# Kernel tuning notes

Measured on AMD Instinct MI355X. Metric: run time of the kernel, lower is better.

## Reference

```python
import jax, jax.numpy as jnp
import numpy as np

GN_GROUPS = 32
GN_EPS = 1e-5


def conv1x1(x, w, b):
    # x: [B,C,H,W], w: [O,C], b: [O]
    return jnp.einsum('bchw,oc->bohw', x, w) + b[None, :, None, None]


def maxpool2(x):
    B, C, H, W = x.shape
    return x.reshape(B, C, H // 2, 2, W // 2, 2).max(axis=(3, 5))


def group_norm(x, w, b, groups=GN_GROUPS, eps=GN_EPS):
    B, C, H, W = x.shape
    xg = x.reshape(B, groups, -1)
    m = xg.mean(axis=-1, keepdims=True)
    v = xg.var(axis=-1, keepdims=True)
    xn = ((xg - m) * jax.lax.rsqrt(v + eps)).reshape(B, C, H, W)
    return xn * w[None, :, None, None] + b[None, :, None, None]


def setup_inputs() -> dict:
    key = jax.random.key(0)
    ks = jax.random.split(key, 8)
    B, C, Ci, H, W = 4, 128, 64, 96, 96
    s_in = 1.0 / np.sqrt(C)
    s_ic = 1.0 / np.sqrt(Ci)
    return {
        'x': jax.random.normal(ks[0], (B, C, H, W), jnp.float32),
        'w_theta': jax.random.normal(ks[1], (Ci, C), jnp.float32) * s_in,
        'b_theta': jnp.zeros((Ci,), jnp.float32),
        'w_phi': jax.random.normal(ks[2], (Ci, C), jnp.float32) * s_in,
        'b_phi': jnp.zeros((Ci,), jnp.float32),
        'w_g': jax.random.normal(ks[3], (Ci, C), jnp.float32) * s_in,
        'b_g': jnp.zeros((Ci,), jnp.float32),
        'w_W': jax.random.normal(ks[4], (C, Ci), jnp.float32) * s_ic,
        'b_W': jnp.zeros((C,), jnp.float32),
        'gn_w': jnp.ones((C,), jnp.float32),
        'gn_b': jnp.zeros((C,), jnp.float32),
    }


def reference(x, w_theta, b_theta, w_phi, b_phi, w_g, b_g, w_W, b_W, gn_w, gn_b):
    B, C, H, W = x.shape
    Ci = w_theta.shape[0]
    # projections (1x1 convs); phi and g are 2x2 max-pooled (sub_sample=True)
    theta = conv1x1(x, w_theta, b_theta).reshape(B, Ci, H * W)          # [B,Ci,N]
    phi = maxpool2(conv1x1(x, w_phi, b_phi)).reshape(B, Ci, -1)         # [B,Ci,N']
    g = maxpool2(conv1x1(x, w_g, b_g)).reshape(B, Ci, -1)               # [B,Ci,N']
    # unscaled single-head attention
    f = jnp.einsum('bcn,bcm->bnm', theta, phi)                          # [B,N,N']
    f = jax.nn.softmax(f, axis=-1)
    y = jnp.einsum('bnm,bcm->bcn', f, g).reshape(B, Ci, H, W)           # [B,Ci,H,W]
    w_y = group_norm(conv1x1(y, w_W, b_W), gn_w, gn_b)
    return w_y + x
```

## Files before the change

### kernel.cpp

```cpp
#include <hip/hip_runtime.h>
#include <math.h>

#define B_ 4
#define C_ 128
#define CI_ 64
#define H_ 96
#define W_ 96
#define HW_ (H_*W_)
#define NP_ 2304
#define GROUPS_ 32
#define EPS_ 1e-5f
#define KVT_ 32
#define NT_ (NP_/KVT_)

typedef _Float16 f16x8 __attribute__((ext_vector_type(8)));
typedef _Float16 f16x2 __attribute__((ext_vector_type(2)));
typedef __attribute__((ext_vector_type(4))) float f32x4;

__device__ inline f32x4 mfma16h(f16x8 a, f16x8 b, f32x4 c) {
    return __builtin_amdgcn_mfma_f32_16x16x32_f16(a, b, c, 0, 0, 0);
}
__device__ inline float h2f(unsigned short s) {
    return (float)__builtin_bit_cast(_Float16, s);
}
__device__ inline unsigned pk_f16(float a, float b) {
    return __builtin_bit_cast(unsigned, __builtin_amdgcn_cvt_pkrtz(a, b));
}
__device__ inline f16x8 pk8(float v0, float v1, float v2, float v3,
                            float v4, float v5, float v6, float v7) {
    uint4 u = { pk_f16(v0, v1), pk_f16(v2, v3), pk_f16(v4, v5), pk_f16(v6, v7) };
    return __builtin_bit_cast(f16x8, u);
}
__device__ inline void gload_lds16(const void* g, void* l) {
    __builtin_amdgcn_global_load_lds(
        (const __attribute__((address_space(1))) void*)reinterpret_cast<uintptr_t>(g),
        (__attribute__((address_space(3))) void*)(unsigned)reinterpret_cast<uintptr_t>(l),
        16, 0, 0);
}

__global__ __launch_bounds__(256) void wprep_kernel(
    const float* __restrict__ w_theta, const float* __restrict__ w_phi,
    const float* __restrict__ w_g,     const float* __restrict__ w_W,
    unsigned short* __restrict__ Whall)
{
    const int idx = blockIdx.x * 256 + threadIdx.x;
    float v;
    if      (idx <  8192) v = w_theta[idx];
    else if (idx < 16384) v = w_phi[idx - 8192];
    else if (idx < 24576) v = w_g[idx - 16384];
    else                  v = w_W[idx - 24576];
    Whall[idx] = __builtin_bit_cast(unsigned short, (_Float16)v);
}

__global__ __launch_bounds__(256) void proj_kernel(
    const float* __restrict__ x, const unsigned short* __restrict__ Whall,
    const float* __restrict__ b_theta, const float* __restrict__ b_phi,
    const float* __restrict__ b_g,
    unsigned short* __restrict__ Qo, unsigned short* __restrict__ phiF,
    unsigned short* __restrict__ gF)
{
    __shared__ __align__(16) unsigned short pb[4][16 * 72];

    const int t    = threadIdx.x;
    const int wv   = t >> 6;
    const int lane = t & 63;
    const int lr   = lane & 15;
    const int lg   = lane >> 4;
    const int b    = blockIdx.y;
    const int px0  = blockIdx.x * 64 + wv * 16;

    const float* xb = x + (size_t)b * C_ * HW_ + px0 + lr;
    f16x8 xa[4];
    #pragma unroll
    for (int u = 0; u < 4; ++u) {
        const float* p = xb + (size_t)(u * 32 + lg * 8) * HW_;
        xa[u] = pk8(p[0], p[(size_t)HW_], p[2 * (size_t)HW_], p[3 * (size_t)HW_],
                    p[4 * (size_t)HW_], p[5 * (size_t)HW_], p[6 * (size_t)HW_],
                    p[7 * (size_t)HW_]);
    }

    #pragma unroll
    for (int mat = 0; mat < 3; ++mat) {
        const unsigned short* Whp = Whall + mat * 8192;
        const float* bsel = (mat == 0) ? b_theta : (mat == 1) ? b_phi : b_g;
        unsigned short* osel = (mat == 0) ? Qo : (mat == 1) ? phiF : gF;

        f32x4 D[4];
        #pragma unroll
        for (int ct = 0; ct < 4; ++ct) D[ct] = (f32x4){0.f, 0.f, 0.f, 0.f};
        #pragma unroll
        for (int u = 0; u < 4; ++u)
            #pragma unroll
            for (int ct = 0; ct < 4; ++ct) {
                f16x8 wb = *(const f16x8*)&Whp[(ct * 16 + lr) * 128 + u * 32 + lg * 8];
                D[ct] = mfma16h(xa[u], wb, D[ct]);
            }

        #pragma unroll
        for (int ct = 0; ct < 4; ++ct) {
            const float bi = bsel[ct * 16 + lr];
            #pragma unroll
            for (int r2 = 0; r2 < 4; ++r2)
                pb[wv][(4 * lg + r2) * 72 + ct * 16 + lr] =
                    __builtin_bit_cast(unsigned short, (_Float16)(D[ct][r2] + bi));
        }
        {
            const int px = lane >> 2, ch = lane & 3;
            f16x8 y0 = *(const f16x8*)&pb[wv][px * 72 + ch * 16];
            f16x8 y1 = *(const f16x8*)&pb[wv][px * 72 + ch * 16 + 8];
            unsigned short* op = osel + ((size_t)b * HW_ + px0 + px) * CI_ + ch * 16;
            *(f16x8*)op       = y0;
            *(f16x8*)(op + 8) = y1;
        }
    }
}

__global__ __launch_bounds__(256) void pool_kernel(
    const unsigned short* __restrict__ phiF, const unsigned short* __restrict__ gF,
    unsigned short* __restrict__ Ko, unsigned short* __restrict__ Vt)
{
    const int t   = threadIdx.x;
    const int b   = blockIdx.y;
    const int mat = blockIdx.z;
    const int idx = blockIdx.x * 256 + t;
    int m, ci;
    if (mat == 0) { m = idx >> 6; ci = idx & 63; }
    else          { ci = idx / NP_; m = idx - ci * NP_; }
    const int ph = m / 48, pw = m % 48;
    const int n00 = (ph * 2) * W_ + pw * 2;
    const unsigned short* src = mat ? gF : phiF;
    const unsigned short* p = src + ((size_t)b * HW_ + n00) * CI_ + ci;
    float v = fmaxf(fmaxf(h2f(p[0]), h2f(p[CI_])),
                    fmaxf(h2f(p[(size_t)W_ * CI_]), h2f(p[(size_t)(W_ + 1) * CI_])));
    unsigned short r = __builtin_bit_cast(unsigned short, (_Float16)v);
    if (mat == 0) {
        Ko[((size_t)b * NP_ + m) * CI_ + ci] = r;
    } else {
        const int ms = (m & ~31) | (8 * ((m >> 2) & 3) + 4 * ((m >> 4) & 1) + (m & 3));
        Vt[((size_t)b * CI_ + ci) * NP_ + ms] = r;
    }
}

__global__ __launch_bounds__(128) void attn_kernel(
    const unsigned short* __restrict__ Qg, const unsigned short* __restrict__ Kg,
    const unsigned short* __restrict__ Vt, unsigned short* __restrict__ Yh)
{
    __shared__ unsigned char Klds[2][4096];
    __shared__ unsigned char Vlds[2][4096];

    const int t    = threadIdx.x;
    const int wv   = t >> 6;
    const int lane = t & 63;
    const int lr   = lane & 15;
    const int lg   = lane >> 4;
    const int b    = blockIdx.y;
    const int q0   = blockIdx.x * 32 + wv * 16;

    const int krow = lane >> 3;
    const int kchk = (lane & 7) ^ krow;
    const int vrow = lane >> 2;
    const int vchk = (lane & 3) ^ (vrow & 3);

    const unsigned short* Kb = Kg + (size_t)b * NP_ * CI_;
    const unsigned short* Vb = Vt + (size_t)b * CI_ * NP_;

    f16x8 qf[2];
    #pragma unroll
    for (int u = 0; u < 2; ++u)
        qf[u] = *(const f16x8*)(Qg + ((size_t)b * HW_ + q0 + lr) * CI_ + u * 32 + lg * 8);

    f32x4 o_acc[4];
    #pragma unroll
    for (int dt = 0; dt < 4; ++dt) o_acc[dt] = (f32x4){0.f, 0.f, 0.f, 0.f};
    float mrun = -1e30f, lrun = 0.f;

#define STAGE(BUF, TT)                                                          \
    {                                                                           \
        const int kv0_ = (TT) * KVT_;                                           \
        if (wv == 0) {                                                          \
            _Pragma("unroll")                                                   \
            for (int i = 0; i < 4; ++i)                                         \
                gload_lds16(Kb + (size_t)(kv0_ + 8 * i + krow) * CI_ + kchk * 8,\
                            &Klds[BUF][i * 1024]);                              \
        } else {                                                                \
            _Pragma("unroll")                                                   \
            for (int i = 0; i < 4; ++i)                                         \
                gload_lds16(Vb + (size_t)(16 * i + vrow) * NP_ + kv0_ + vchk * 8,\
                            &Vlds[BUF][i * 1024]);                              \
        }                                                                       \
    }

#define COMPUTE(BUF)                                                            \
    {                                                                           \
        f16x8 kf[2][2];                                                         \
        _Pragma("unroll")                                                       \
        for (int u = 0; u < 2; ++u)                                             \
            _Pragma("unroll")                                                   \
            for (int k4 = 0; k4 < 2; ++k4)                                      \
                kf[u][k4] = *(const f16x8*)&Klds[BUF][(k4 * 16 + lr) * 128      \
                                + (((4 * u + lg) ^ (lr & 7)) << 4)];            \
        f32x4 s[2];                                                             \
        s[0] = (f32x4){0.f, 0.f, 0.f, 0.f};                                     \
        s[1] = (f32x4){0.f, 0.f, 0.f, 0.f};                                     \
        __builtin_amdgcn_s_setprio(1);                                          \
        _Pragma("unroll")                                                       \
        for (int u = 0; u < 2; ++u) {                                           \
            s[0] = mfma16h(kf[u][0], qf[u], s[0]);                              \
            s[1] = mfma16h(kf[u][1], qf[u], s[1]);                              \
        }                                                                       \
        __builtin_amdgcn_s_setprio(0);                                          \
        float tmax = fmaxf(fmaxf(fmaxf(s[0][0], s[0][1]),                       \
                                 fmaxf(s[0][2], s[0][3])),                      \
                           fmaxf(fmaxf(s[1][0], s[1][1]),                       \
                                 fmaxf(s[1][2], s[1][3])));                     \
        if (!__all(tmax <= mrun + 8.0f)) {                                      \
            tmax = fmaxf(tmax, __shfl_xor(tmax, 16));                           \
            tmax = fmaxf(tmax, __shfl_xor(tmax, 32));                           \
            const float mnew = fmaxf(mrun, tmax);                               \
            const float sc = __expf(mrun - mnew);                               \
            lrun *= sc;                                                         \
            _Pragma("unroll")                                                   \
            for (int r2 = 0; r2 < 4; ++r2) {                                    \
                const float scb = __shfl(sc, 4 * lg + r2);                      \
                _Pragma("unroll")                                               \
                for (int dt = 0; dt < 4; ++dt) o_acc[dt][r2] *= scb;            \
            }                                                                   \
            mrun = mnew;                                                        \
        }                                                                       \
        const float e00 = __expf(s[0][0] - mrun);                               \
        const float e01 = __expf(s[0][1] - mrun);                               \
        const float e02 = __expf(s[0][2] - mrun);                               \
        const float e03 = __expf(s[0][3] - mrun);                               \
        const float e10 = __expf(s[1][0] - mrun);                               \
        const float e11 = __expf(s[1][1] - mrun);                               \
        const float e12 = __expf(s[1][2] - mrun);                               \
        const float e13 = __expf(s[1][3] - mrun);                               \
        lrun += ((e00 + e01) + (e02 + e03)) + ((e10 + e11) + (e12 + e13));      \
        f16x8 pf = pk8(e00, e01, e02, e03, e10, e11, e12, e13);                 \
        __builtin_amdgcn_s_setprio(1);                                          \
        _Pragma("unroll")                                                       \
        for (int dt = 0; dt < 4; ++dt) {                                        \
            const int vrow_ = dt * 16 + lr;                                     \
            f16x8 vf = *(const f16x8*)&Vlds[BUF][vrow_ * 64                     \
                            + (((lg ^ (lr & 3))) << 4)];                        \
            o_acc[dt] = mfma16h(pf, vf, o_acc[dt]);                             \
        }                                                                       \
        __builtin_amdgcn_s_setprio(0);                                          \
    }

    STAGE(0, 0);
    STAGE(1, 1);

    for (int it = 0; it < NT_ / 2; ++it) {
        const int t0 = 2 * it;
        asm volatile("s_waitcnt vmcnt(4)" ::: "memory");
        __builtin_amdgcn_s_barrier();
        COMPUTE(0);
        __builtin_amdgcn_s_barrier();
        if (t0 + 2 < NT_) STAGE(0, t0 + 2);
        if (it == NT_ / 2 - 1) {
            asm volatile("s_waitcnt vmcnt(0)" ::: "memory");
        } else {
            asm volatile("s_waitcnt vmcnt(4)" ::: "memory");
        }
        __builtin_amdgcn_s_barrier();
        COMPUTE(1);
        __builtin_amdgcn_s_barrier();
        if (t0 + 3 < NT_) STAGE(1, t0 + 3);
    }

    float lt = lrun;
    lt += __shfl_xor(lt, 16);
    lt += __shfl_xor(lt, 32);
    unsigned short* yb = (unsigned short*)&Klds[wv][0];
    #pragma unroll
    for (int r2 = 0; r2 < 4; ++r2) {
        const float inv = 1.0f / __shfl(lt, 4 * lg + r2);
        #pragma unroll
        for (int dt = 0; dt < 4; ++dt)
            yb[(4 * lg + r2) * 72 + dt * 16 + lr] =
                __builtin_bit_cast(unsigned short, (_Float16)(o_acc[dt][r2] * inv));
    }
    {
        const int px = lane >> 2, ch = lane & 3;
        f16x8 y0 = *(const f16x8*)&yb[px * 72 + ch * 16];
        f16x8 y1 = *(const f16x8*)&yb[px * 72 + ch * 16 + 8];
        unsigned short* op = Yh + ((size_t)b * HW_ + q0 + px) * CI_ + ch * 16;
        *(f16x8*)op       = y0;
        *(f16x8*)(op + 8) = y1;
    }
#undef STAGE
#undef COMPUTE
}

__global__ __launch_bounds__(256) void conv2_kernel(
    const unsigned short* __restrict__ Yh, const unsigned short* __restrict__ wWh,
    const float* __restrict__ bW, float* __restrict__ Zg, float* __restrict__ gpart)
{
    __shared__ float wpart[4][32][2];

    const int t    = threadIdx.x;
    const int wv   = t >> 6;
    const int lane = t & 63;
    const int lr   = lane & 15;
    const int lg   = lane >> 4;
    const int b    = blockIdx.y;
    const int n0   = blockIdx.x * 64 + wv * 16;

    f16x8 ya[2];
    #pragma unroll
    for (int u = 0; u < 2; ++u)
        ya[u] = *(const f16x8*)(Yh + ((size_t)b * HW_ + n0 + lr) * CI_ + u * 32 + lg * 8);

    float* Zb = Zg + (size_t)b * C_ * HW_ + n0 + lr;
    #pragma unroll
    for (int ot = 0; ot < 8; ++ot) {
        f32x4 D = (f32x4){0.f, 0.f, 0.f, 0.f};
        #pragma unroll
        for (int u = 0; u < 2; ++u) {
            f16x8 wa = *(const f16x8*)&wWh[(ot * 16 + lr) * CI_ + u * 32 + lg * 8];
            D = mfma16h(wa, ya[u], D);
        }
        float zs = 0.f, zq = 0.f;
        #pragma unroll
        for (int r2 = 0; r2 < 4; ++r2) {
            const int o = ot * 16 + 4 * lg + r2;
            const float z = D[r2] + bW[o];
            Zb[(size_t)o * HW_] = z;
            zs += z;
            zq += z * z;
        }
        zs += __shfl_xor(zs, 1);  zq += __shfl_xor(zq, 1);
        zs += __shfl_xor(zs, 2);  zq += __shfl_xor(zq, 2);
        zs += __shfl_xor(zs, 4);  zq += __shfl_xor(zq, 4);
        zs += __shfl_xor(zs, 8);  zq += __shfl_xor(zq, 8);
        if (lr == 0) {
            wpart[wv][ot * 4 + lg][0] = zs;
            wpart[wv][ot * 4 + lg][1] = zq;
        }
    }
    __syncthreads();
    if (t < 64) {
        const int g = t >> 1, w = t & 1;
        const float v = wpart[0][g][w] + wpart[1][g][w]
                      + wpart[2][g][w] + wpart[3][g][w];
        gpart[(((size_t)b * 144 + blockIdx.x) * 32 + g) * 2 + w] = v;
    }
}

__global__ __launch_bounds__(256) void final_kernel(
    const float* __restrict__ Zg, const float* __restrict__ xg,
    const float* __restrict__ gpart, const float* __restrict__ gnw,
    const float* __restrict__ gnb, float* __restrict__ out)
{
    __shared__ float red[256][2];
    const int t = threadIdx.x;
    const int c = blockIdx.x;
    const int b = blockIdx.y;
    const int g = c >> 2;

    float v1 = 0.f, v2 = 0.f;
    if (t < 144) {
        v1 = gpart[(((size_t)b * 144 + t) * 32 + g) * 2 + 0];
        v2 = gpart[(((size_t)b * 144 + t) * 32 + g) * 2 + 1];
    }
    red[t][0] = v1; red[t][1] = v2;
    __syncthreads();
    for (int off = 128; off > 0; off >>= 1) {
        if (t < off) { red[t][0] += red[t + off][0]; red[t][1] += red[t + off][1]; }
        __syncthreads();
    }
    const float invn = 1.0f / (4 * HW_);
    const float mean = red[0][0] * invn;
    const float var  = red[0][1] * invn - mean * mean;
    const float rstd = rsqrtf(var + EPS_);
    const float sc = rstd * gnw[c];
    const float sh = gnb[c] - mean * sc;

    const float4* zp = (const float4*)(Zg + ((size_t)b * C_ + c) * HW_);
    const float4* xp = (const float4*)(xg + ((size_t)b * C_ + c) * HW_);
    float4*       op = (float4*)(out + ((size_t)b * C_ + c) * HW_);
    #pragma unroll
    for (int i = 0; i < HW_ / 4 / 256; ++i) {
        const int j = i * 256 + t;
        const float4 z  = zp[j];
        const float4 xv = xp[j];
        float4 o;
        o.x = z.x * sc + sh + xv.x;
        o.y = z.y * sc + sh + xv.y;
        o.z = z.z * sc + sh + xv.z;
        o.w = z.w * sc + sh + xv.w;
        op[j] = o;
    }
}

extern "C" void kernel_launch(void* const* d_in, const int* in_sizes, int n_in,
                              void* d_out, int out_size, void* d_ws, size_t ws_size,
                              hipStream_t stream)
{
    const float* x       = (const float*)d_in[0];
    const float* w_theta = (const float*)d_in[1];
    const float* b_theta = (const float*)d_in[2];
    const float* w_phi   = (const float*)d_in[3];
    const float* b_phi   = (const float*)d_in[4];
    const float* w_g     = (const float*)d_in[5];
    const float* b_g     = (const float*)d_in[6];
    const float* w_W     = (const float*)d_in[7];
    const float* b_W     = (const float*)d_in[8];
    const float* gn_w    = (const float*)d_in[9];
    const float* gn_b    = (const float*)d_in[10];
    float* out = (float*)d_out;
    char* wsb  = (char*)d_ws;

    unsigned short* Q    = (unsigned short*)(wsb);
    unsigned short* K    = (unsigned short*)(wsb +  4718592);
    unsigned short* Vt   = (unsigned short*)(wsb +  5898240);
    unsigned short* phiF = (unsigned short*)(wsb +  7077888);
    unsigned short* gF   = (unsigned short*)(wsb + 11796480);
    unsigned short* Yh   = (unsigned short*)(wsb +  7077888);
    float* gpart         = (float*)(wsb + 11796480);
    float* Z             = (float*)(wsb + 16515072);
    unsigned short* Whall= (unsigned short*)(wsb + 35390464);
    unsigned short* wWh  = Whall + 24576;

    wprep_kernel<<<128, 256, 0, stream>>>(w_theta, w_phi, w_g, w_W, Whall);
    proj_kernel <<<dim3(HW_ / 64, B_), 256, 0, stream>>>(
        x, Whall, b_theta, b_phi, b_g, Q, phiF, gF);
    pool_kernel <<<dim3(NP_ * CI_ / 256, B_, 2), 256, 0, stream>>>(phiF, gF, K, Vt);
    attn_kernel <<<dim3(HW_ / 32, B_), 128, 0, stream>>>(Q, K, Vt, Yh);
    conv2_kernel<<<dim3(HW_ / 64, B_), 256, 0, stream>>>(Yh, wWh, b_W, Z, gpart);
    final_kernel<<<dim3(C_, B_), 256, 0, stream>>>(Z, x, gpart, gn_w, gn_b, out);
}
```

Before: 117.0 us.

## Split attention KV range across wave pairs and store conv output as fp16

The attention kernel now runs 256 threads per block. Two wave pairs each handle half of the pooled key/value sequence (36 tiles each) for the same 32 queries. The partial softmax states (running max, sum, output) are merged through LDS at the end, a split-K style flash-decoding combine that shortens each wave's serial loop and adds parallelism. Separately, the conv output Z is stored as fp16 instead of fp32, which halves the traffic between conv2 and the final GroupNorm kernel at some cost in precision.

```diff
diff --git a/kernel.cpp b/kernel.cpp
--- a/kernel.cpp
+++ b/kernel.cpp
@@ -12,6 +12,7 @@
 #define EPS_ 1e-5f
 #define KVT_ 32
 #define NT_ (NP_/KVT_)
+#define TPH_ 36
 
 typedef _Float16 f16x8 __attribute__((ext_vector_type(8)));
 typedef _Float16 f16x2 __attribute__((ext_vector_type(2)));
@@ -141,20 +142,21 @@
     }
 }
 
-__global__ __launch_bounds__(128) void attn_kernel(
+__global__ __launch_bounds__(256) void attn_kernel(
     const unsigned short* __restrict__ Qg, const unsigned short* __restrict__ Kg,
     const unsigned short* __restrict__ Vt, unsigned short* __restrict__ Yh)
 {
-    __shared__ unsigned char Klds[2][4096];
-    __shared__ unsigned char Vlds[2][4096];
+    __shared__ __align__(16) unsigned char KV[2][2][2][4096];
 
     const int t    = threadIdx.x;
     const int wv   = t >> 6;
+    const int qh   = wv >> 1;
+    const int p    = wv & 1;
     const int lane = t & 63;
     const int lr   = lane & 15;
     const int lg   = lane >> 4;
     const int b    = blockIdx.y;
-    const int q0   = blockIdx.x * 32 + wv * 16;
+    const int q0   = blockIdx.x * 32;
 
     const int krow = lane >> 3;
     const int kchk = (lane & 7) ^ krow;
@@ -167,26 +169,27 @@
     f16x8 qf[2];
     #pragma unroll
     for (int u = 0; u < 2; ++u)
-        qf[u] = *(const f16x8*)(Qg + ((size_t)b * HW_ + q0 + lr) * CI_ + u * 32 + lg * 8);
+        qf[u] = *(const f16x8*)(Qg
+            + ((size_t)b * HW_ + q0 + qh * 16 + lr) * CI_ + u * 32 + lg * 8);
 
     f32x4 o_acc[4];
     #pragma unroll
     for (int dt = 0; dt < 4; ++dt) o_acc[dt] = (f32x4){0.f, 0.f, 0.f, 0.f};
     float mrun = -1e30f, lrun = 0.f;
 
-#define STAGE(BUF, TT)                                                          \
+#define STAGE(BUF, TL)                                                          \
     {                                                                           \
-        const int kv0_ = (TT) * KVT_;                                           \
-        if (wv == 0) {                                                          \
+        const int kv0_ = (p * TPH_ + (TL)) * KVT_;                              \
+        if (qh == 0) {                                                          \
             _Pragma("unroll")                                                   \
             for (int i = 0; i < 4; ++i)                                         \
                 gload_lds16(Kb + (size_t)(kv0_ + 8 * i + krow) * CI_ + kchk * 8,\
-                            &Klds[BUF][i * 1024]);                              \
+                            &KV[p][BUF][0][i * 1024]);                          \
         } else {                                                                \
             _Pragma("unroll")                                                   \
             for (int i = 0; i < 4; ++i)                                         \
                 gload_lds16(Vb + (size_t)(16 * i + vrow) * NP_ + kv0_ + vchk * 8,\
-                            &Vlds[BUF][i * 1024]);                              \
+                            &KV[p][BUF][1][i * 1024]);                          \
         }                                                                       \
     }
 
@@ -197,7 +200,7 @@
         for (int u = 0; u < 2; ++u)                                             \
             _Pragma("unroll")                                                   \
             for (int k4 = 0; k4 < 2; ++k4)                                      \
-                kf[u][k4] = *(const f16x8*)&Klds[BUF][(k4 * 16 + lr) * 128      \
+                kf[u][k4] = *(const f16x8*)&KV[p][BUF][0][(k4 * 16 + lr) * 128  \
                                 + (((4 * u + lg) ^ (lr & 7)) << 4)];            \
         f32x4 s[2];                                                             \
         s[0] = (f32x4){0.f, 0.f, 0.f, 0.f};                                     \
@@ -241,7 +244,7 @@
         _Pragma("unroll")                                                       \
         for (int dt = 0; dt < 4; ++dt) {                                        \
             const int vrow_ = dt * 16 + lr;                                     \
-            f16x8 vf = *(const f16x8*)&Vlds[BUF][vrow_ * 64                     \
+            f16x8 vf = *(const f16x8*)&KV[p][BUF][1][vrow_ * 64                 \
                             + (((lg ^ (lr & 3))) << 4)];                        \
             o_acc[dt] = mfma16h(pf, vf, o_acc[dt]);                             \
         }                                                                       \
@@ -251,14 +254,14 @@
     STAGE(0, 0);
     STAGE(1, 1);
 
-    for (int it = 0; it < NT_ / 2; ++it) {
+    for (int it = 0; it < TPH_ / 2; ++it) {
         const int t0 = 2 * it;
         asm volatile("s_waitcnt vmcnt(4)" ::: "memory");
         __builtin_amdgcn_s_barrier();
         COMPUTE(0);
         __builtin_amdgcn_s_barrier();
-        if (t0 + 2 < NT_) STAGE(0, t0 + 2);
-        if (it == NT_ / 2 - 1) {
+        if (t0 + 2 < TPH_) STAGE(0, t0 + 2);
+        if (it == TPH_ / 2 - 1) {
             asm volatile("s_waitcnt vmcnt(0)" ::: "memory");
         } else {
             asm volatile("s_waitcnt vmcnt(4)" ::: "memory");
@@ -266,28 +269,51 @@
         __builtin_amdgcn_s_barrier();
         COMPUTE(1);
         __builtin_amdgcn_s_barrier();
-        if (t0 + 3 < NT_) STAGE(1, t0 + 3);
-    }
+        if (t0 + 3 < TPH_) STAGE(1, t0 + 3);
+    }
+
+    float* cb   = (float*)&KV[0][0][0][0];
+    float* Olds = cb;
+    float* mlb  = cb + 2 * 32 * 68;
 
     float lt = lrun;
     lt += __shfl_xor(lt, 16);
     lt += __shfl_xor(lt, 32);
-    unsigned short* yb = (unsigned short*)&Klds[wv][0];
-    #pragma unroll
-    for (int r2 = 0; r2 < 4; ++r2) {
-        const float inv = 1.0f / __shfl(lt, 4 * lg + r2);
-        #pragma unroll
-        for (int dt = 0; dt < 4; ++dt)
-            yb[(4 * lg + r2) * 72 + dt * 16 + lr] =
-                __builtin_bit_cast(unsigned short, (_Float16)(o_acc[dt][r2] * inv));
-    }
+    if (lg == 0) {
+        mlb[(p * 32 + qh * 16 + lr) * 2 + 0] = mrun;
+        mlb[(p * 32 + qh * 16 + lr) * 2 + 1] = lt;
+    }
+    __syncthreads();
+
     {
-        const int px = lane >> 2, ch = lane & 3;
-        f16x8 y0 = *(const f16x8*)&yb[px * 72 + ch * 16];
-        f16x8 y1 = *(const f16x8*)&yb[px * 72 + ch * 16 + 8];
-        unsigned short* op = Yh + ((size_t)b * HW_ + q0 + px) * CI_ + ch * 16;
-        *(f16x8*)op       = y0;
-        *(f16x8*)(op + 8) = y1;
+        const int row = qh * 16 + lr;
+        const float mg = fmaxf(mlb[(row) * 2 + 0], mlb[(32 + row) * 2 + 0]);
+        const float fac = __expf(mrun - mg);
+        #pragma unroll
+        for (int r2 = 0; r2 < 4; ++r2) {
+            const float fb = __shfl(fac, 4 * lg + r2);
+            #pragma unroll
+            for (int dt = 0; dt < 4; ++dt)
+                Olds[(p * 32 + qh * 16 + 4 * lg + r2) * 68 + dt * 16 + lr]
+                    = o_acc[dt][r2] * fb;
+        }
+    }
+    __syncthreads();
+
+    {
+        const int row = t >> 3;
+        const int c0  = (t & 7) * 8;
+        const float m0 = mlb[row * 2 + 0],  l0 = mlb[row * 2 + 1];
+        const float m1 = mlb[(32 + row) * 2 + 0], l1 = mlb[(32 + row) * 2 + 1];
+        const float mg = fmaxf(m0, m1);
+        const float inv = 1.0f / (l0 * __expf(m0 - mg) + l1 * __expf(m1 - mg));
+        const float* o0 = &Olds[row * 68 + c0];
+        const float* o1 = &Olds[(32 + row) * 68 + c0];
+        float a[8];
+        #pragma unroll
+        for (int i = 0; i < 8; ++i) a[i] = (o0[i] + o1[i]) * inv;
+        f16x8 y = pk8(a[0], a[1], a[2], a[3], a[4], a[5], a[6], a[7]);
+        *(f16x8*)(Yh + ((size_t)b * HW_ + q0 + row) * CI_ + c0) = y;
     }
 #undef STAGE
 #undef COMPUTE
@@ -295,7 +321,8 @@
 
 __global__ __launch_bounds__(256) void conv2_kernel(
     const unsigned short* __restrict__ Yh, const unsigned short* __restrict__ wWh,
-    const float* __restrict__ bW, float* __restrict__ Zg, float* __restrict__ gpart)
+    const float* __restrict__ bW, unsigned short* __restrict__ Zh,
+    float* __restrict__ gpart)
 {
     __shared__ float wpart[4][32][2];
 
@@ -312,7 +339,7 @@
     for (int u = 0; u < 2; ++u)
         ya[u] = *(const f16x8*)(Yh + ((size_t)b * HW_ + n0 + lr) * CI_ + u * 32 + lg * 8);
 
-    float* Zb = Zg + (size_t)b * C_ * HW_ + n0 + lr;
+    unsigned short* Zb = Zh + (size_t)b * C_ * HW_ + n0 + lr;
     #pragma unroll
     for (int ot = 0; ot < 8; ++ot) {
         f32x4 D = (f32x4){0.f, 0.f, 0.f, 0.f};
@@ -326,7 +353,7 @@
         for (int r2 = 0; r2 < 4; ++r2) {
             const int o = ot * 16 + 4 * lg + r2;
             const float z = D[r2] + bW[o];
-            Zb[(size_t)o * HW_] = z;
+            Zb[(size_t)o * HW_] = __builtin_bit_cast(unsigned short, (_Float16)z);
             zs += z;
             zq += z * z;
         }
@@ -349,7 +376,7 @@
 }
 
 __global__ __launch_bounds__(256) void final_kernel(
-    const float* __restrict__ Zg, const float* __restrict__ xg,
+    const unsigned short* __restrict__ Zh, const float* __restrict__ xg,
     const float* __restrict__ gpart, const float* __restrict__ gnw,
     const float* __restrict__ gnb, float* __restrict__ out)
 {
@@ -377,19 +404,19 @@
     const float sc = rstd * gnw[c];
     const float sh = gnb[c] - mean * sc;
 
-    const float4* zp = (const float4*)(Zg + ((size_t)b * C_ + c) * HW_);
+    const unsigned short* zp = Zh + ((size_t)b * C_ + c) * HW_;
     const float4* xp = (const float4*)(xg + ((size_t)b * C_ + c) * HW_);
     float4*       op = (float4*)(out + ((size_t)b * C_ + c) * HW_);
     #pragma unroll
     for (int i = 0; i < HW_ / 4 / 256; ++i) {
         const int j = i * 256 + t;
-        const float4 z  = zp[j];
+        const ushort4 zv = *(const ushort4*)(zp + (size_t)j * 4);
         const float4 xv = xp[j];
         float4 o;
-        o.x = z.x * sc + sh + xv.x;
-        o.y = z.y * sc + sh + xv.y;
-        o.z = z.z * sc + sh + xv.z;
-        o.w = z.w * sc + sh + xv.w;
+        o.x = h2f(zv.x) * sc + sh + xv.x;
+        o.y = h2f(zv.y) * sc + sh + xv.y;
+        o.z = h2f(zv.z) * sc + sh + xv.z;
+        o.w = h2f(zv.w) * sc + sh + xv.w;
         op[j] = o;
     }
 }
@@ -419,7 +446,7 @@
     unsigned short* gF   = (unsigned short*)(wsb + 11796480);
     unsigned short* Yh   = (unsigned short*)(wsb +  7077888);
     float* gpart         = (float*)(wsb + 11796480);
-    float* Z             = (float*)(wsb + 16515072);
+    unsigned short* Zh   = (unsigned short*)(wsb + 16515072);
     unsigned short* Whall= (unsigned short*)(wsb + 35390464);
     unsigned short* wWh  = Whall + 24576;
 
@@ -427,7 +454,7 @@
     proj_kernel <<<dim3(HW_ / 64, B_), 256, 0, stream>>>(
         x, Whall, b_theta, b_phi, b_g, Q, phiF, gF);
     pool_kernel <<<dim3(NP_ * CI_ / 256, B_, 2), 256, 0, stream>>>(phiF, gF, K, Vt);
-    attn_kernel <<<dim3(HW_ / 32, B_), 128, 0, stream>>>(Q, K, Vt, Yh);
-    conv2_kernel<<<dim3(HW_ / 64, B_), 256, 0, stream>>>(Yh, wWh, b_W, Z, gpart);
-    final_kernel<<<dim3(C_, B_), 256, 0, stream>>>(Z, x, gpart, gn_w, gn_b, out);
-}
+    attn_kernel <<<dim3(HW_ / 32, B_), 256, 0, stream>>>(Q, K, Vt, Yh);
+    conv2_kernel<<<dim3(HW_ / 64, B_), 256, 0, stream>>>(Yh, wWh, b_W, Zh, gpart);
+    final_kernel<<<dim3(C_, B_), 256, 0, stream>>>(Zh, x, gpart, gn_w, gn_b, out);
+}
```

Measured after the change: 118.5 us. About the same (+1.3%).

## Double attention KV tile to 64 and store conv2 output in fp16

Applied to the files above, without the earlier changes.

The attention kernel now stages 64 keys and values per tile instead of 32. It uses a unified 128-byte-row XOR swizzle for K and V in LDS and issues four QK and two PV MFMAs per tile, which halves the number of barriers and online-softmax rescale checks. Separately, the pre-GroupNorm conv output Z is written as fp16 rather than fp32, halving its write and read traffic between conv2 and the final kernel. Costs are doubled LDS use per block, which may lower occupancy, and extra rounding error in Z before normalization.

```diff
diff --git a/kernel.cpp b/kernel.cpp
--- a/kernel.cpp
+++ b/kernel.cpp
@@ -10,8 +10,8 @@
 #define NP_ 2304
 #define GROUPS_ 32
 #define EPS_ 1e-5f
-#define KVT_ 32
-#define NT_ (NP_/KVT_)
+#define KVT_ 64
+#define NTT_ (NP_/KVT_)
 
 typedef _Float16 f16x8 __attribute__((ext_vector_type(8)));
 typedef _Float16 f16x2 __attribute__((ext_vector_type(2)));
@@ -145,8 +145,8 @@
     const unsigned short* __restrict__ Qg, const unsigned short* __restrict__ Kg,
     const unsigned short* __restrict__ Vt, unsigned short* __restrict__ Yh)
 {
-    __shared__ unsigned char Klds[2][4096];
-    __shared__ unsigned char Vlds[2][4096];
+    __shared__ __align__(16) unsigned char Klds[2][8192];
+    __shared__ __align__(16) unsigned char Vlds[2][8192];
 
     const int t    = threadIdx.x;
     const int wv   = t >> 6;
@@ -156,10 +156,8 @@
     const int b    = blockIdx.y;
     const int q0   = blockIdx.x * 32 + wv * 16;
 
-    const int krow = lane >> 3;
-    const int kchk = (lane & 7) ^ krow;
-    const int vrow = lane >> 2;
-    const int vchk = (lane & 3) ^ (vrow & 3);
+    const int srow = lane >> 3;
+    const int schk = (lane & 7) ^ srow;
 
     const unsigned short* Kb = Kg + (size_t)b * NP_ * CI_;
     const unsigned short* Vb = Vt + (size_t)b * CI_ * NP_;
@@ -179,40 +177,42 @@
         const int kv0_ = (TT) * KVT_;                                           \
         if (wv == 0) {                                                          \
             _Pragma("unroll")                                                   \
-            for (int i = 0; i < 4; ++i)                                         \
-                gload_lds16(Kb + (size_t)(kv0_ + 8 * i + krow) * CI_ + kchk * 8,\
+            for (int i = 0; i < 8; ++i)                                         \
+                gload_lds16(Kb + (size_t)(kv0_ + 8 * i + srow) * CI_ + schk * 8,\
                             &Klds[BUF][i * 1024]);                              \
         } else {                                                                \
             _Pragma("unroll")                                                   \
-            for (int i = 0; i < 4; ++i)                                         \
-                gload_lds16(Vb + (size_t)(16 * i + vrow) * NP_ + kv0_ + vchk * 8,\
+            for (int i = 0; i < 8; ++i)                                         \
+                gload_lds16(Vb + (size_t)(8 * i + srow) * NP_ + kv0_ + schk * 8,\
                             &Vlds[BUF][i * 1024]);                              \
         }                                                                       \
     }
 
 #define COMPUTE(BUF)                                                            \
     {                                                                           \
-        f16x8 kf[2][2];                                                         \
+        f16x8 kf[2][4];                                                         \
         _Pragma("unroll")                                                       \
         for (int u = 0; u < 2; ++u)                                             \
             _Pragma("unroll")                                                   \
-            for (int k4 = 0; k4 < 2; ++k4)                                      \
+            for (int k4 = 0; k4 < 4; ++k4)                                      \
                 kf[u][k4] = *(const f16x8*)&Klds[BUF][(k4 * 16 + lr) * 128      \
                                 + (((4 * u + lg) ^ (lr & 7)) << 4)];            \
-        f32x4 s[2];                                                             \
-        s[0] = (f32x4){0.f, 0.f, 0.f, 0.f};                                     \
-        s[1] = (f32x4){0.f, 0.f, 0.f, 0.f};                                     \
+        f32x4 s[4];                                                             \
+        _Pragma("unroll")                                                       \
+        for (int k4 = 0; k4 < 4; ++k4) s[k4] = (f32x4){0.f, 0.f, 0.f, 0.f};     \
         __builtin_amdgcn_s_setprio(1);                                          \
         _Pragma("unroll")                                                       \
-        for (int u = 0; u < 2; ++u) {                                           \
-            s[0] = mfma16h(kf[u][0], qf[u], s[0]);                              \
-            s[1] = mfma16h(kf[u][1], qf[u], s[1]);                              \
+        for (int u = 0; u < 2; ++u)                                             \
+            _Pragma("unroll")                                                   \
+            for (int k4 = 0; k4 < 4; ++k4)                                      \
+                s[k4] = mfma16h(kf[u][k4], qf[u], s[k4]);                       \
+        __builtin_amdgcn_s_setprio(0);                                          \
+        float tmax = s[0][0];                                                   \
+        _Pragma("unroll")                                                       \
+        for (int k4 = 0; k4 < 4; ++k4) {                                        \
+            tmax = fmaxf(tmax, fmaxf(fmaxf(s[k4][0], s[k4][1]),                 \
+                                     fmaxf(s[k4][2], s[k4][3])));               \
         }                                                                       \
-        __builtin_amdgcn_s_setprio(0);                                          \
-        float tmax = fmaxf(fmaxf(fmaxf(s[0][0], s[0][1]),                       \
-                                 fmaxf(s[0][2], s[0][3])),                      \
-                           fmaxf(fmaxf(s[1][0], s[1][1]),                       \
-                                 fmaxf(s[1][2], s[1][3])));                     \
         if (!__all(tmax <= mrun + 8.0f)) {                                      \
             tmax = fmaxf(tmax, __shfl_xor(tmax, 16));                           \
             tmax = fmaxf(tmax, __shfl_xor(tmax, 32));                           \
@@ -227,23 +227,31 @@
             }                                                                   \
             mrun = mnew;                                                        \
         }                                                                       \
-        const float e00 = __expf(s[0][0] - mrun);                               \
-        const float e01 = __expf(s[0][1] - mrun);                               \
-        const float e02 = __expf(s[0][2] - mrun);                               \
-        const float e03 = __expf(s[0][3] - mrun);                               \
-        const float e10 = __expf(s[1][0] - mrun);                               \
-        const float e11 = __expf(s[1][1] - mrun);                               \
-        const float e12 = __expf(s[1][2] - mrun);                               \
-        const float e13 = __expf(s[1][3] - mrun);                               \
-        lrun += ((e00 + e01) + (e02 + e03)) + ((e10 + e11) + (e12 + e13));      \
-        f16x8 pf = pk8(e00, e01, e02, e03, e10, e11, e12, e13);                 \
+        unsigned pw[8];                                                         \
+        _Pragma("unroll")                                                       \
+        for (int k4 = 0; k4 < 4; ++k4) {                                        \
+            const float a0 = __expf(s[k4][0] - mrun);                           \
+            const float a1 = __expf(s[k4][1] - mrun);                           \
+            const float a2 = __expf(s[k4][2] - mrun);                           \
+            const float a3 = __expf(s[k4][3] - mrun);                           \
+            lrun += (a0 + a1) + (a2 + a3);                                      \
+            pw[k4 * 2]     = pk_f16(a0, a1);                                    \
+            pw[k4 * 2 + 1] = pk_f16(a2, a3);                                    \
+        }                                                                       \
+        const f16x8 pf0 = __builtin_bit_cast(f16x8,                             \
+            (uint4){pw[0], pw[1], pw[2], pw[3]});                               \
+        const f16x8 pf1 = __builtin_bit_cast(f16x8,                             \
+            (uint4){pw[4], pw[5], pw[6], pw[7]});                               \
         __builtin_amdgcn_s_setprio(1);                                          \
         _Pragma("unroll")                                                       \
         for (int dt = 0; dt < 4; ++dt) {                                        \
-            const int vrow_ = dt * 16 + lr;                                     \
-            f16x8 vf = *(const f16x8*)&Vlds[BUF][vrow_ * 64                     \
-                            + (((lg ^ (lr & 3))) << 4)];                        \
-            o_acc[dt] = mfma16h(pf, vf, o_acc[dt]);                             \
+            const int vb_ = (dt * 16 + lr) * 128;                               \
+            f16x8 vf0 = *(const f16x8*)&Vlds[BUF][vb_                           \
+                            + (((lg) ^ (lr & 7)) << 4)];                        \
+            f16x8 vf1 = *(const f16x8*)&Vlds[BUF][vb_                           \
+                            + (((4 + lg) ^ (lr & 7)) << 4)];                    \
+            o_acc[dt] = mfma16h(pf0, vf0, o_acc[dt]);                           \
+            o_acc[dt] = mfma16h(pf1, vf1, o_acc[dt]);                           \
         }                                                                       \
         __builtin_amdgcn_s_setprio(0);                                          \
     }
@@ -251,28 +259,28 @@
     STAGE(0, 0);
     STAGE(1, 1);
 
-    for (int it = 0; it < NT_ / 2; ++it) {
+    for (int it = 0; it < NTT_ / 2; ++it) {
         const int t0 = 2 * it;
-        asm volatile("s_waitcnt vmcnt(4)" ::: "memory");
+        asm volatile("s_waitcnt vmcnt(8)" ::: "memory");
         __builtin_amdgcn_s_barrier();
         COMPUTE(0);
         __builtin_amdgcn_s_barrier();
-        if (t0 + 2 < NT_) STAGE(0, t0 + 2);
-        if (it == NT_ / 2 - 1) {
+        if (t0 + 2 < NTT_) STAGE(0, t0 + 2);
+        if (it == NTT_ / 2 - 1) {
             asm volatile("s_waitcnt vmcnt(0)" ::: "memory");
         } else {
-            asm volatile("s_waitcnt vmcnt(4)" ::: "memory");
+            asm volatile("s_waitcnt vmcnt(8)" ::: "memory");
         }
         __builtin_amdgcn_s_barrier();
         COMPUTE(1);
         __builtin_amdgcn_s_barrier();
-        if (t0 + 3 < NT_) STAGE(1, t0 + 3);
+        if (t0 + 3 < NTT_) STAGE(1, t0 + 3);
     }
 
     float lt = lrun;
     lt += __shfl_xor(lt, 16);
     lt += __shfl_xor(lt, 32);
-    unsigned short* yb = (unsigned short*)&Klds[wv][0];
+    unsigned short* yb = (unsigned short*)&Klds[0][wv * 2304];
     #pragma unroll
     for (int r2 = 0; r2 < 4; ++r2) {
         const float inv = 1.0f / __shfl(lt, 4 * lg + r2);
@@ -295,7 +303,8 @@
 
 __global__ __launch_bounds__(256) void conv2_kernel(
     const unsigned short* __restrict__ Yh, const unsigned short* __restrict__ wWh,
-    const float* __restrict__ bW, float* __restrict__ Zg, float* __restrict__ gpart)
+    const float* __restrict__ bW, unsigned short* __restrict__ Zh,
+    float* __restrict__ gpart)
 {
     __shared__ float wpart[4][32][2];
 
@@ -312,7 +321,7 @@
     for (int u = 0; u < 2; ++u)
         ya[u] = *(const f16x8*)(Yh + ((size_t)b * HW_ + n0 + lr) * CI_ + u * 32 + lg * 8);
 
-    float* Zb = Zg + (size_t)b * C_ * HW_ + n0 + lr;
+    unsigned short* Zb = Zh + (size_t)b * C_ * HW_ + n0 + lr;
     #pragma unroll
     for (int ot = 0; ot < 8; ++ot) {
         f32x4 D = (f32x4){0.f, 0.f, 0.f, 0.f};
@@ -326,7 +335,7 @@
         for (int r2 = 0; r2 < 4; ++r2) {
             const int o = ot * 16 + 4 * lg + r2;
             const float z = D[r2] + bW[o];
-            Zb[(size_t)o * HW_] = z;
+            Zb[(size_t)o * HW_] = __builtin_bit_cast(unsigned short, (_Float16)z);
             zs += z;
             zq += z * z;
         }
@@ -349,7 +358,7 @@
 }
 
 __global__ __launch_bounds__(256) void final_kernel(
-    const float* __restrict__ Zg, const float* __restrict__ xg,
+    const unsigned short* __restrict__ Zh, const float* __restrict__ xg,
     const float* __restrict__ gpart, const float* __restrict__ gnw,
     const float* __restrict__ gnb, float* __restrict__ out)
 {
@@ -377,19 +386,19 @@
     const float sc = rstd * gnw[c];
     const float sh = gnb[c] - mean * sc;
 
-    const float4* zp = (const float4*)(Zg + ((size_t)b * C_ + c) * HW_);
+    const unsigned short* zp = Zh + ((size_t)b * C_ + c) * HW_;
     const float4* xp = (const float4*)(xg + ((size_t)b * C_ + c) * HW_);
     float4*       op = (float4*)(out + ((size_t)b * C_ + c) * HW_);
     #pragma unroll
     for (int i = 0; i < HW_ / 4 / 256; ++i) {
         const int j = i * 256 + t;
-        const float4 z  = zp[j];
+        const ushort4 zv = *(const ushort4*)(zp + (size_t)j * 4);
         const float4 xv = xp[j];
         float4 o;
-        o.x = z.x * sc + sh + xv.x;
-        o.y = z.y * sc + sh + xv.y;
-        o.z = z.z * sc + sh + xv.z;
-        o.w = z.w * sc + sh + xv.w;
+        o.x = h2f(zv.x) * sc + sh + xv.x;
+        o.y = h2f(zv.y) * sc + sh + xv.y;
+        o.z = h2f(zv.z) * sc + sh + xv.z;
+        o.w = h2f(zv.w) * sc + sh + xv.w;
         op[j] = o;
     }
 }
@@ -419,7 +428,7 @@
     unsigned short* gF   = (unsigned short*)(wsb + 11796480);
     unsigned short* Yh   = (unsigned short*)(wsb +  7077888);
     float* gpart         = (float*)(wsb + 11796480);
-    float* Z             = (float*)(wsb + 16515072);
+    unsigned short* Zh   = (unsigned short*)(wsb + 16515072);
     unsigned short* Whall= (unsigned short*)(wsb + 35390464);
     unsigned short* wWh  = Whall + 24576;
 
@@ -428,6 +437,6 @@
         x, Whall, b_theta, b_phi, b_g, Q, phiF, gF);
     pool_kernel <<<dim3(NP_ * CI_ / 256, B_, 2), 256, 0, stream>>>(phiF, gF, K, Vt);
     attn_kernel <<<dim3(HW_ / 32, B_), 128, 0, stream>>>(Q, K, Vt, Yh);
-    conv2_kernel<<<dim3(HW_ / 64, B_), 256, 0, stream>>>(Yh, wWh, b_W, Z, gpart);
-    final_kernel<<<dim3(C_, B_), 256, 0, stream>>>(Z, x, gpart, gn_w, gn_b, out);
-}
+    conv2_kernel<<<dim3(HW_ / 64, B_), 256, 0, stream>>>(Yh, wWh, b_W, Zh, gpart);
+    final_kernel<<<dim3(C_, B_), 256, 0, stream>>>(Zh, x, gpart, gn_w, gn_b, out);
+}
```

Measured after the change: 122.8 us. 1.05x slower.
